# Performance work log

Measured on AMD Instinct MI355X. Metric: run time of the kernel, lower is better.

The kernel has to match this reference:

```python
import jax, jax.numpy as jnp
import numpy as np

NUM_STEPS = 5


def setup_inputs() -> dict:
    key = jax.random.key(0)
    ks = jax.random.split(key, 12)
    B, N, H, E, A = 8, 1024, 64, 2, 8
    initial_state = jax.random.normal(ks[0], (B, N, H), dtype=jnp.float32)
    annotation = jax.random.normal(ks[1], (B, N, A), dtype=jnp.float32)
    # sparse-ish positive adjacency, scaled so matmul outputs don't saturate gates
    adj_matrix = jax.random.uniform(ks[2], (B, N, 2 * N * E), dtype=jnp.float32) * 0.01
    s = 0.05
    W_edge = jax.random.normal(ks[3], (H, H * E), dtype=jnp.float32) * s
    b_edge = jax.random.normal(ks[4], (H * E,), dtype=jnp.float32) * s
    W_gate = jax.random.normal(ks[5], (3 * H, H), dtype=jnp.float32) * s
    b_gate = jax.random.normal(ks[6], (H,), dtype=jnp.float32) * s
    W_hid = jax.random.normal(ks[7], (H + A, H), dtype=jnp.float32) * s
    b_hid = jax.random.normal(ks[8], (H,), dtype=jnp.float32) * s
    W_out = jax.random.normal(ks[9], (H, 1), dtype=jnp.float32) * s
    b_out = jax.random.normal(ks[10], (1,), dtype=jnp.float32) * s
    return dict(initial_state=initial_state, annotation=annotation, adj_matrix=adj_matrix,
                W_edge=W_edge, b_edge=b_edge, W_gate=W_gate, b_gate=b_gate,
                W_hid=W_hid, b_hid=b_hid, W_out=W_out, b_out=b_out)


def reference(initial_state, annotation, adj_matrix, W_edge, b_edge,
              W_gate, b_gate, W_hid, b_hid, W_out, b_out):
    B, N, H = initial_state.shape
    E = W_edge.shape[1] // H
    boundary = N * E
    A_in = adj_matrix[:, :, :boundary]   # [B, N, N*E]
    A_out = adj_matrix[:, :, boundary:]  # [B, N, N*E]

    h = initial_state
    for _ in range(NUM_STEPS):
        # Linear(H, H*E) then view/transpose to [B, N*E, H].
        # Original computes incoming_edge and outgoing_edge with the SAME
        # linear on the SAME input -> identical tensors; compute once.
        edge = jnp.einsum('bnh,he->bne', h, W_edge) + b_edge      # [B, N, H*E]
        edge = edge.reshape(B, N, H, E).transpose(0, 3, 1, 2).reshape(B, N * E, H)
        a_in = jnp.matmul(A_in, edge)    # [B, N, H]
        a_out = jnp.matmul(A_out, edge)  # [B, N, H]
        a = jnp.concatenate([a_in, a_out, h], axis=2)             # [B, N, 3H]
        # update and reset use the same gate linear -> equal; compute once.
        z = jax.nn.sigmoid(jnp.einsum('bnk,kh->bnh', a, W_gate) + b_gate)
        a_r = jnp.concatenate([a_in, a_out, z * h], axis=2)
        h_tilde = jnp.tanh(jnp.einsum('bnk,kh->bnh', a_r, W_gate) + b_gate)
        h = (1.0 - z) * h + z * h_tilde

    # task_id not in {18, 19}: node-level output head
    ha = jnp.concatenate([h, annotation], axis=2)                 # [B, N, H+A]
    out = jnp.tanh(jnp.einsum('bnk,kh->bnh', ha, W_hid) + b_hid)  # [B, N, H]
    out = (jnp.einsum('bnh,ho->bno', out, W_out) + b_out).sum(axis=2)  # [B, N]
    return out
```

## Files before the change

### kernel.cpp

```cpp
#include <hip/hip_runtime.h>
#include <math.h>

#define BN    8
#define NN    1024
#define HH    64
#define ADIM  8
#define STEPS 5
#define K2    2048
#define ROWS  (BN*NN)

typedef __attribute__((ext_vector_type(8))) short bf16x8;
typedef __attribute__((ext_vector_type(4))) float f32x4;

__device__ __forceinline__ unsigned short f2bf(float f) {
    unsigned int u = __float_as_uint(f);
    u += 0x7FFF + ((u >> 16) & 1);
    return (unsigned short)(u >> 16);
}
__device__ __forceinline__ float bf2f(unsigned short h) {
    return __uint_as_float(((unsigned int)h) << 16);
}


__global__ __launch_bounds__(256) void conv_adj(
    const float* __restrict__ in, unsigned short* __restrict__ out)
{
    int tid = blockIdx.x * 256 + threadIdx.x;
    int r   = tid >> 7;
    int dkb = tid & 127;
    int b = r >> 10, n = r & 1023;
    int dir = dkb >> 6, kb = dkb & 63;
    const float* src = in + ((size_t)r << 12) + (dkb << 5);
    unsigned short* dst = out
        + ((((((size_t)b * 2 + dir) * 64 + kb) * 64 + (n >> 4)) << 4) + (n & 15)) * 32;
    #pragma unroll
    for (int i = 0; i < 8; ++i) {
        float4 v = ((const float4*)src)[i];
        ushort4 o;
        o.x = f2bf(v.x); o.y = f2bf(v.y); o.z = f2bf(v.z); o.w = f2bf(v.w);
        ((ushort4*)dst)[i] = o;
    }
}

__global__ __launch_bounds__(256) void prep_pack(
    const float* __restrict__ Wg, const float* __restrict__ We,
    unsigned short* __restrict__ wgp, unsigned short* __restrict__ wep)
{
    int t = blockIdx.x * 256 + threadIdx.x;
    if (t < 12288) {
        int k = t >> 6, c = t & 63;
        float v = Wg[t];
        unsigned short hi = f2bf(v);
        unsigned short lo = f2bf(v - bf2f(hi));
        wgp[(size_t)c * 192 + k] = hi;
        wgp[(size_t)(64 + c) * 192 + k] = lo;
    } else if (t < 20480) {
        int u = t - 12288;
        int k = u >> 7, c = u & 127;
        float v = We[u];
        unsigned short hi = f2bf(v);
        unsigned short lo = f2bf(v - bf2f(hi));
        wep[(size_t)c * 64 + k] = hi;
        wep[(size_t)(128 + c) * 64 + k] = lo;
    }
}

__device__ __forceinline__ size_t edge_addr(int b, int h, int k) {
    int kb = k >> 5, hb = h >> 4;
    return (((size_t)b * 64 + kb) * 4 + hb) * 512
         + (size_t)(h & 15) * 32 + (k & 31);
}

__global__ __launch_bounds__(256) void init_kernel(
    const float* __restrict__ init_state,
    const float* __restrict__ We, const float* __restrict__ be,
    float* __restrict__ h_ws, unsigned short* __restrict__ edge_t)
{
    __shared__ float h_lds[4][65];
    int t = threadIdx.x;
    int r = t >> 6, hp = t & 63;
    int row = blockIdx.x * 4 + r;
    float hv = init_state[(size_t)row * 64 + hp];
    h_ws[(size_t)row * 64 + hp] = hv;
    h_lds[r][hp] = hv;
    __syncthreads();
    int b = row >> 10, n = row & 1023;
    #pragma unroll
    for (int e = 0; e < 2; ++e) {
        float acc = be[hp * 2 + e];
        #pragma unroll 8
        for (int c = 0; c < 64; ++c)
            acc += h_lds[r][c] * We[c * 128 + hp * 2 + e];
        edge_t[edge_addr(b, hp, e * NN + n)] = f2bf(acc);
    }
}

__global__ __launch_bounds__(512) void step_kernel(
    const unsigned short* __restrict__ adjf,
    const unsigned short* __restrict__ ein,
    unsigned short* __restrict__ eout,
    float* __restrict__ h_ws,
    const unsigned short* __restrict__ wgp,
    const unsigned short* __restrict__ wep,
    const float* __restrict__ bg,
    const float* __restrict__ be,
    int do_edge)
{
    __shared__ __attribute__((aligned(16))) unsigned short Xhi[32][200];
    __shared__ __attribute__((aligned(16))) unsigned short Xlo[32][200];
    __shared__ __attribute__((aligned(16))) float          hf [32][68];
    __shared__ __attribute__((aligned(16))) unsigned short HNhi[32][72];
    __shared__ __attribute__((aligned(16))) unsigned short HNlo[32][72];
    __shared__ __attribute__((aligned(16))) float          red[4][16][68];

    int t  = threadIdx.x;
    int b  = blockIdx.x >> 5;
    int mt = blockIdx.x & 31;
    int n0 = mt * 32;
    size_t hbase = ((size_t)(b * NN + n0)) * 64;

    {
        int r = t >> 4, cg = (t & 15) * 4;
        float4 v = *(const float4*)(h_ws + hbase + (size_t)r * 64 + cg);
        float vv[4] = {v.x, v.y, v.z, v.w};
        #pragma unroll
        for (int j = 0; j < 4; ++j) {
            float hv = vv[j];
            unsigned short hi = f2bf(hv), lo = f2bf(hv - bf2f(hi));
            Xhi[r][128 + cg + j] = hi;
            Xlo[r][128 + cg + j] = lo;
            hf[r][cg + j] = hv;
        }
    }

    int lane = t & 63, w = t >> 6, l15 = lane & 15, q = lane >> 4;
    int dir = w >> 2, rh = (w >> 1) & 1, kc = w & 1;
    int nb  = mt * 2 + rh;
    int loff = l15 * 32 + q * 8;

    const unsigned short* Ap = adjf
        + ((((size_t)(b * 2 + dir) * 64 + kc * 32) * 64 + nb) * 512) + loff;
    const unsigned short* Bp = ein
        + (((size_t)b * 64 + kc * 32) * 4) * 512 + loff;

    f32x4 acc[4];
    #pragma unroll
    for (int ct = 0; ct < 4; ++ct) acc[ct] = (f32x4){0.f, 0.f, 0.f, 0.f};

    #pragma unroll 4
    for (int kb = 0; kb < 32; ++kb) {
        bf16x8 af = *(const bf16x8*)(Ap + kb * 32768);
        #pragma unroll
        for (int ct = 0; ct < 4; ++ct) {
            bf16x8 bfr = *(const bf16x8*)(Bp + kb * 2048 + ct * 512);
            acc[ct] = __builtin_amdgcn_mfma_f32_16x16x32_bf16(af, bfr, acc[ct], 0, 0, 0);
        }
    }

    int gg = w >> 1;
    if (kc == 1) {
        #pragma unroll
        for (int ct = 0; ct < 4; ++ct)
            #pragma unroll
            for (int i = 0; i < 4; ++i)
                red[gg][q * 4 + i][ct * 16 + l15] = acc[ct][i];
    }
    __syncthreads();
    if (kc == 0) {
        #pragma unroll
        for (int ct = 0; ct < 4; ++ct)
            #pragma unroll
            for (int i = 0; i < 4; ++i) {
                float v = acc[ct][i] + red[gg][q * 4 + i][ct * 16 + l15];
                unsigned short hi = f2bf(v), lo = f2bf(v - bf2f(hi));
                int r  = rh * 16 + q * 4 + i;
                int cc = dir * 64 + ct * 16 + l15;
                Xhi[r][cc] = hi;
                Xlo[r][cc] = lo;
            }
    }
    __syncthreads();

    int mg = w & 1, cg16 = w >> 1;
    int arow = mg * 16 + l15;
    int cc = cg16 * 16 + l15;
    const unsigned short* wcol = wgp + (size_t)cc * 192;
    f32x4 as = (f32x4){0.f, 0.f, 0.f, 0.f}, az;

    #pragma unroll
    for (int ks = 0; ks < 4; ++ks) {
        bf16x8 ah = *(const bf16x8*)&Xhi[arow][ks * 32 + q * 8];
        bf16x8 al = *(const bf16x8*)&Xlo[arow][ks * 32 + q * 8];
        const unsigned short* wb = wcol + ks * 32 + q * 8;
        bf16x8 bh = *(const bf16x8*)wb;
        bf16x8 bl = *(const bf16x8*)(wb + 64 * 192);
        as = __builtin_amdgcn_mfma_f32_16x16x32_bf16(ah, bh, as, 0, 0, 0);
        as = __builtin_amdgcn_mfma_f32_16x16x32_bf16(ah, bl, as, 0, 0, 0);
        as = __builtin_amdgcn_mfma_f32_16x16x32_bf16(al, bh, as, 0, 0, 0);
    }
    az = as;
    #pragma unroll
    for (int ks = 4; ks < 6; ++ks) {
        bf16x8 ah = *(const bf16x8*)&Xhi[arow][ks * 32 + q * 8];
        bf16x8 al = *(const bf16x8*)&Xlo[arow][ks * 32 + q * 8];
        const unsigned short* wb = wcol + ks * 32 + q * 8;
        bf16x8 bh = *(const bf16x8*)wb;
        bf16x8 bl = *(const bf16x8*)(wb + 64 * 192);
        az = __builtin_amdgcn_mfma_f32_16x16x32_bf16(ah, bh, az, 0, 0, 0);
        az = __builtin_amdgcn_mfma_f32_16x16x32_bf16(ah, bl, az, 0, 0, 0);
        az = __builtin_amdgcn_mfma_f32_16x16x32_bf16(al, bh, az, 0, 0, 0);
    }
    __syncthreads();

    float zv[4], hv[4];
    float bgv = bg[cc];
    #pragma unroll
    for (int i = 0; i < 4; ++i) {
        int r = mg * 16 + q * 4 + i;
        float z = 1.f / (1.f + __expf(-(az[i] + bgv)));
        float h = hf[r][cc];
        zv[i] = z; hv[i] = h;
        float zh = z * h;
        unsigned short hi = f2bf(zh), lo = f2bf(zh - bf2f(hi));
        Xhi[r][128 + cc] = hi;
        Xlo[r][128 + cc] = lo;
    }
    __syncthreads();

    #pragma unroll
    for (int ks = 4; ks < 6; ++ks) {
        bf16x8 ah = *(const bf16x8*)&Xhi[arow][ks * 32 + q * 8];
        bf16x8 al = *(const bf16x8*)&Xlo[arow][ks * 32 + q * 8];
        const unsigned short* wb = wcol + ks * 32 + q * 8;
        bf16x8 bh = *(const bf16x8*)wb;
        bf16x8 bl = *(const bf16x8*)(wb + 64 * 192);
        as = __builtin_amdgcn_mfma_f32_16x16x32_bf16(ah, bh, as, 0, 0, 0);
        as = __builtin_amdgcn_mfma_f32_16x16x32_bf16(ah, bl, as, 0, 0, 0);
        as = __builtin_amdgcn_mfma_f32_16x16x32_bf16(al, bh, as, 0, 0, 0);
    }

    #pragma unroll
    for (int i = 0; i < 4; ++i) {
        int r = mg * 16 + q * 4 + i;
        float ht = tanhf(as[i] + bgv);
        float z  = zv[i];
        float hn = (1.f - z) * hv[i] + z * ht;
        h_ws[hbase + (size_t)r * 64 + cc] = hn;
        if (do_edge) {
            unsigned short hi = f2bf(hn), lo = f2bf(hn - bf2f(hi));
            HNhi[r][cc] = hi;
            HNlo[r][cc] = lo;
        }
    }
    if (!do_edge) return;
    __syncthreads();

    int me = w & 1, cb2 = (w >> 1) * 2;
    int erow = me * 16 + l15;
    f32x4 ae[2];
    ae[0] = ae[1] = (f32x4){0.f, 0.f, 0.f, 0.f};
    #pragma unroll
    for (int ks = 0; ks < 2; ++ks) {
        bf16x8 ah = *(const bf16x8*)&HNhi[erow][ks * 32 + q * 8];
        bf16x8 al = *(const bf16x8*)&HNlo[erow][ks * 32 + q * 8];
        #pragma unroll
        for (int p = 0; p < 2; ++p) {
            int ec = (cb2 + p) * 16 + l15;
            const unsigned short* wb = wep + (size_t)ec * 64 + ks * 32 + q * 8;
            bf16x8 bh = *(const bf16x8*)wb;
            bf16x8 bl = *(const bf16x8*)(wb + 128 * 64);
            ae[p] = __builtin_amdgcn_mfma_f32_16x16x32_bf16(ah, bh, ae[p], 0, 0, 0);
            ae[p] = __builtin_amdgcn_mfma_f32_16x16x32_bf16(ah, bl, ae[p], 0, 0, 0);
            ae[p] = __builtin_amdgcn_mfma_f32_16x16x32_bf16(al, bh, ae[p], 0, 0, 0);
        }
    }
    #pragma unroll
    for (int p = 0; p < 2; ++p) {
        int ec = (cb2 + p) * 16 + l15;
        float bev = be[ec];
        int h = ec >> 1, e = ec & 1;
        int k = e * NN + n0 + me * 16 + q * 4;
        ushort4 ev;
        ev.x = f2bf(ae[p][0] + bev);
        ev.y = f2bf(ae[p][1] + bev);
        ev.z = f2bf(ae[p][2] + bev);
        ev.w = f2bf(ae[p][3] + bev);
        *(ushort4*)(eout + edge_addr(b, h, k)) = ev;
    }
}

__global__ __launch_bounds__(256) void head_kernel(
    const float* __restrict__ h_ws, const float* __restrict__ ann,
    const float* __restrict__ Wh, const float* __restrict__ bh,
    const float* __restrict__ Wo, const float* __restrict__ bo,
    float* __restrict__ out)
{
    __shared__ float Wh_l[72 * 64];
    __shared__ float ha[4][72];
    int t = threadIdx.x;
    #pragma unroll
    for (int l = 0; l < 18; ++l) {
        int idx = t + l * 256;
        Wh_l[idx] = Wh[idx];
    }
    int r = t >> 6, hp = t & 63;
    int row = blockIdx.x * 4 + r;
    ha[r][hp] = h_ws[(size_t)row * 64 + hp];
    if (hp < ADIM) ha[r][64 + hp] = ann[(size_t)row * ADIM + hp];
    __syncthreads();

    float acc = bh[hp];
    #pragma unroll 8
    for (int k = 0; k < 72; ++k)
        acc += ha[r][k] * Wh_l[k * 64 + hp];
    float v = tanhf(acc) * Wo[hp];
    #pragma unroll
    for (int o = 32; o; o >>= 1) v += __shfl_down(v, o, 64);
    if (hp == 0) out[row] = v + bo[0];
}

extern "C" void kernel_launch(void* const* d_in, const int* in_sizes, int n_in,
                              void* d_out, int out_size, void* d_ws, size_t ws_size,
                              hipStream_t stream) {
    const float* init_state = (const float*)d_in[0];
    const float* ann = (const float*)d_in[1];
    const float* adj = (const float*)d_in[2];
    const float* We  = (const float*)d_in[3];
    const float* be  = (const float*)d_in[4];
    const float* Wg  = (const float*)d_in[5];
    const float* bg  = (const float*)d_in[6];
    const float* Wh  = (const float*)d_in[7];
    const float* bh  = (const float*)d_in[8];
    const float* Wo  = (const float*)d_in[9];
    const float* bo  = (const float*)d_in[10];
    float* out = (float*)d_out;

    char* wsb = (char*)d_ws;
    unsigned short* adj_f  = (unsigned short*)wsb;
    unsigned short* edge_a = (unsigned short*)(wsb + 67108864);
    unsigned short* edge_b = (unsigned short*)(wsb + 69206016);
    float*          h_ws   = (float*)(wsb + 71303168);
    unsigned short* wgp    = (unsigned short*)(wsb + 73400320);
    unsigned short* wep    = (unsigned short*)(wsb + 73449472);

    conv_adj<<<dim3(4096), dim3(256), 0, stream>>>(adj, adj_f);
    prep_pack<<<dim3(80), dim3(256), 0, stream>>>(Wg, We, wgp, wep);
    init_kernel<<<dim3(ROWS / 4), dim3(256), 0, stream>>>(init_state, We, be, h_ws, edge_a);
    for (int s = 0; s < STEPS; ++s) {
        const unsigned short* ein = (s & 1) ? edge_b : edge_a;
        unsigned short* eo        = (s & 1) ? edge_a : edge_b;
        step_kernel<<<dim3(256), dim3(512), 0, stream>>>(
            adj_f, ein, eo, h_ws, wgp, wep, bg, be, (s < STEPS - 1) ? 1 : 0);
    }
    head_kernel<<<dim3(ROWS / 4), dim3(256), 0, stream>>>(h_ws, ann, Wh, bh, Wo, bo, out);
}
```

Before: 429.8 us.

## Merge prep kernels, fuse head into last step, use row-major adjacency layout

Combines the adjacency conversion, weight packing and initial edge computation into one launch, and fuses the output head into the final GRU step so h no longer round-trips through global memory for a separate head kernel. The adjacency bf16 copy moves from a tiled MFMA-fragment layout to plain row-major, which makes the conversion a straight streaming cast but gives the step kernel strided per-row fragment loads instead of contiguous tile loads. tanhf is swapped for an exp-based fast tanh. The trade-off is launch-count and layout-transform savings against possibly worse load coalescing in the main matmul loop.

```diff
diff --git a/kernel.cpp b/kernel.cpp
--- a/kernel.cpp
+++ b/kernel.cpp
@@ -20,83 +20,79 @@
 __device__ __forceinline__ float bf2f(unsigned short h) {
     return __uint_as_float(((unsigned int)h) << 16);
 }
-
-
-__global__ __launch_bounds__(256) void conv_adj(
-    const float* __restrict__ in, unsigned short* __restrict__ out)
-{
-    int tid = blockIdx.x * 256 + threadIdx.x;
-    int r   = tid >> 7;
-    int dkb = tid & 127;
-    int b = r >> 10, n = r & 1023;
-    int dir = dkb >> 6, kb = dkb & 63;
-    const float* src = in + ((size_t)r << 12) + (dkb << 5);
-    unsigned short* dst = out
-        + ((((((size_t)b * 2 + dir) * 64 + kb) * 64 + (n >> 4)) << 4) + (n & 15)) * 32;
-    #pragma unroll
-    for (int i = 0; i < 8; ++i) {
-        float4 v = ((const float4*)src)[i];
-        ushort4 o;
-        o.x = f2bf(v.x); o.y = f2bf(v.y); o.z = f2bf(v.z); o.w = f2bf(v.w);
-        ((ushort4*)dst)[i] = o;
-    }
-}
-
-__global__ __launch_bounds__(256) void prep_pack(
-    const float* __restrict__ Wg, const float* __restrict__ We,
-    unsigned short* __restrict__ wgp, unsigned short* __restrict__ wep)
-{
-    int t = blockIdx.x * 256 + threadIdx.x;
-    if (t < 12288) {
-        int k = t >> 6, c = t & 63;
-        float v = Wg[t];
-        unsigned short hi = f2bf(v);
-        unsigned short lo = f2bf(v - bf2f(hi));
-        wgp[(size_t)c * 192 + k] = hi;
-        wgp[(size_t)(64 + c) * 192 + k] = lo;
-    } else if (t < 20480) {
-        int u = t - 12288;
-        int k = u >> 7, c = u & 127;
-        float v = We[u];
-        unsigned short hi = f2bf(v);
-        unsigned short lo = f2bf(v - bf2f(hi));
-        wep[(size_t)c * 64 + k] = hi;
-        wep[(size_t)(128 + c) * 64 + k] = lo;
-    }
-}
-
-__device__ __forceinline__ size_t edge_addr(int b, int h, int k) {
-    int kb = k >> 5, hb = h >> 4;
-    return (((size_t)b * 64 + kb) * 4 + hb) * 512
-         + (size_t)(h & 15) * 32 + (k & 31);
-}
-
-__global__ __launch_bounds__(256) void init_kernel(
+__device__ __forceinline__ float ftanh(float x) {
+    float e = __expf(2.f * x);
+    return 1.f - 2.f / (e + 1.f);
+}
+
+__global__ __launch_bounds__(256) void pre_kernel(
+    const float* __restrict__ adj,
     const float* __restrict__ init_state,
     const float* __restrict__ We, const float* __restrict__ be,
-    float* __restrict__ h_ws, unsigned short* __restrict__ edge_t)
+    const float* __restrict__ Wg,
+    unsigned short* __restrict__ adjb,
+    unsigned short* __restrict__ edge_t,
+    float* __restrict__ h_ws,
+    unsigned short* __restrict__ wgp,
+    unsigned short* __restrict__ wep)
 {
     __shared__ float h_lds[4][65];
+    int bid = blockIdx.x;
     int t = threadIdx.x;
-    int r = t >> 6, hp = t & 63;
-    int row = blockIdx.x * 4 + r;
-    float hv = init_state[(size_t)row * 64 + hp];
-    h_ws[(size_t)row * 64 + hp] = hv;
-    h_lds[r][hp] = hv;
-    __syncthreads();
-    int b = row >> 10, n = row & 1023;
-    #pragma unroll
-    for (int e = 0; e < 2; ++e) {
-        float acc = be[hp * 2 + e];
-        #pragma unroll 8
-        for (int c = 0; c < 64; ++c)
-            acc += h_lds[r][c] * We[c * 128 + hp * 2 + e];
-        edge_t[edge_addr(b, hp, e * NN + n)] = f2bf(acc);
+
+    if (bid < 8192) {
+        int tid = bid * 256 + t;
+        #pragma unroll
+        for (int i = 0; i < 4; ++i) {
+            size_t idx = (size_t)tid + (size_t)i * 2097152;
+            float4 v = ((const float4*)adj)[idx];
+            ushort4 o;
+            o.x = f2bf(v.x); o.y = f2bf(v.y); o.z = f2bf(v.z); o.w = f2bf(v.w);
+            ((ushort4*)adjb)[idx] = o;
+        }
+        return;
+    }
+    if (bid < 10240) {
+        int blk = bid - 8192;
+        int r = t >> 6, hp = t & 63;
+        int row = blk * 4 + r;
+        float hv = init_state[(size_t)row * 64 + hp];
+        h_ws[(size_t)row * 64 + hp] = hv;
+        h_lds[r][hp] = hv;
+        __syncthreads();
+        int b = row >> 10, n = row & 1023;
+        #pragma unroll
+        for (int e = 0; e < 2; ++e) {
+            float acc = be[hp * 2 + e];
+            #pragma unroll 8
+            for (int c = 0; c < 64; ++c)
+                acc += h_lds[r][c] * We[c * 128 + hp * 2 + e];
+            edge_t[((size_t)b * 64 + hp) * K2 + e * NN + n] = f2bf(acc);
+        }
+        return;
+    }
+    for (int idx = t; idx < 20480; idx += 256) {
+        if (idx < 12288) {
+            int k = idx >> 6, c = idx & 63;
+            float v = Wg[idx];
+            unsigned short hi = f2bf(v);
+            unsigned short lo = f2bf(v - bf2f(hi));
+            wgp[(size_t)c * 192 + k] = hi;
+            wgp[(size_t)(64 + c) * 192 + k] = lo;
+        } else {
+            int u = idx - 12288;
+            int k = u >> 7, c = u & 127;
+            float v = We[u];
+            unsigned short hi = f2bf(v);
+            unsigned short lo = f2bf(v - bf2f(hi));
+            wep[(size_t)c * 64 + k] = hi;
+            wep[(size_t)(128 + c) * 64 + k] = lo;
+        }
     }
 }
 
 __global__ __launch_bounds__(512) void step_kernel(
-    const unsigned short* __restrict__ adjf,
+    const unsigned short* __restrict__ adjb,
     const unsigned short* __restrict__ ein,
     unsigned short* __restrict__ eout,
     float* __restrict__ h_ws,
@@ -104,7 +100,11 @@
     const unsigned short* __restrict__ wep,
     const float* __restrict__ bg,
     const float* __restrict__ be,
-    int do_edge)
+    const float* __restrict__ ann,
+    const float* __restrict__ Wh, const float* __restrict__ bh,
+    const float* __restrict__ Wo, const float* __restrict__ bo,
+    float* __restrict__ out,
+    int mode)
 {
     __shared__ __attribute__((aligned(16))) unsigned short Xhi[32][200];
     __shared__ __attribute__((aligned(16))) unsigned short Xlo[32][200];
@@ -135,24 +135,22 @@
 
     int lane = t & 63, w = t >> 6, l15 = lane & 15, q = lane >> 4;
     int dir = w >> 2, rh = (w >> 1) & 1, kc = w & 1;
-    int nb  = mt * 2 + rh;
-    int loff = l15 * 32 + q * 8;
-
-    const unsigned short* Ap = adjf
-        + ((((size_t)(b * 2 + dir) * 64 + kc * 32) * 64 + nb) * 512) + loff;
-    const unsigned short* Bp = ein
-        + (((size_t)b * 64 + kc * 32) * 4) * 512 + loff;
+
+    const unsigned short* Al = adjb
+        + ((size_t)(b * NN + n0 + rh * 16 + l15)) * 4096 + dir * K2 + kc * 1024 + q * 8;
+    const unsigned short* Bl = ein
+        + ((size_t)b * 64 + l15) * K2 + kc * 1024 + q * 8;
 
     f32x4 acc[4];
     #pragma unroll
     for (int ct = 0; ct < 4; ++ct) acc[ct] = (f32x4){0.f, 0.f, 0.f, 0.f};
 
-    #pragma unroll 4
-    for (int kb = 0; kb < 32; ++kb) {
-        bf16x8 af = *(const bf16x8*)(Ap + kb * 32768);
+    #pragma unroll 8
+    for (int ks = 0; ks < 32; ++ks) {
+        bf16x8 af = *(const bf16x8*)(Al + ks * 32);
         #pragma unroll
         for (int ct = 0; ct < 4; ++ct) {
-            bf16x8 bfr = *(const bf16x8*)(Bp + kb * 2048 + ct * 512);
+            bf16x8 bfr = *(const bf16x8*)(Bl + (size_t)ct * 16 * K2 + ks * 32);
             acc[ct] = __builtin_amdgcn_mfma_f32_16x16x32_bf16(af, bfr, acc[ct], 0, 0, 0);
         }
     }
@@ -174,9 +172,9 @@
                 float v = acc[ct][i] + red[gg][q * 4 + i][ct * 16 + l15];
                 unsigned short hi = f2bf(v), lo = f2bf(v - bf2f(hi));
                 int r  = rh * 16 + q * 4 + i;
-                int cc = dir * 64 + ct * 16 + l15;
-                Xhi[r][cc] = hi;
-                Xlo[r][cc] = lo;
+                int cc2 = dir * 64 + ct * 16 + l15;
+                Xhi[r][cc2] = hi;
+                Xlo[r][cc2] = lo;
             }
     }
     __syncthreads();
@@ -192,11 +190,11 @@
         bf16x8 ah = *(const bf16x8*)&Xhi[arow][ks * 32 + q * 8];
         bf16x8 al = *(const bf16x8*)&Xlo[arow][ks * 32 + q * 8];
         const unsigned short* wb = wcol + ks * 32 + q * 8;
-        bf16x8 bh = *(const bf16x8*)wb;
-        bf16x8 bl = *(const bf16x8*)(wb + 64 * 192);
-        as = __builtin_amdgcn_mfma_f32_16x16x32_bf16(ah, bh, as, 0, 0, 0);
-        as = __builtin_amdgcn_mfma_f32_16x16x32_bf16(ah, bl, as, 0, 0, 0);
-        as = __builtin_amdgcn_mfma_f32_16x16x32_bf16(al, bh, as, 0, 0, 0);
+        bf16x8 bh2 = *(const bf16x8*)wb;
+        bf16x8 bl2 = *(const bf16x8*)(wb + 64 * 192);
+        as = __builtin_amdgcn_mfma_f32_16x16x32_bf16(ah, bh2, as, 0, 0, 0);
+        as = __builtin_amdgcn_mfma_f32_16x16x32_bf16(ah, bl2, as, 0, 0, 0);
+        as = __builtin_amdgcn_mfma_f32_16x16x32_bf16(al, bh2, as, 0, 0, 0);
     }
     az = as;
     #pragma unroll
@@ -204,11 +202,11 @@
         bf16x8 ah = *(const bf16x8*)&Xhi[arow][ks * 32 + q * 8];
         bf16x8 al = *(const bf16x8*)&Xlo[arow][ks * 32 + q * 8];
         const unsigned short* wb = wcol + ks * 32 + q * 8;
-        bf16x8 bh = *(const bf16x8*)wb;
-        bf16x8 bl = *(const bf16x8*)(wb + 64 * 192);
-        az = __builtin_amdgcn_mfma_f32_16x16x32_bf16(ah, bh, az, 0, 0, 0);
-        az = __builtin_amdgcn_mfma_f32_16x16x32_bf16(ah, bl, az, 0, 0, 0);
-        az = __builtin_amdgcn_mfma_f32_16x16x32_bf16(al, bh, az, 0, 0, 0);
+        bf16x8 bh2 = *(const bf16x8*)wb;
+        bf16x8 bl2 = *(const bf16x8*)(wb + 64 * 192);
+        az = __builtin_amdgcn_mfma_f32_16x16x32_bf16(ah, bh2, az, 0, 0, 0);
+        az = __builtin_amdgcn_mfma_f32_16x16x32_bf16(ah, bl2, az, 0, 0, 0);
+        az = __builtin_amdgcn_mfma_f32_16x16x32_bf16(al, bh2, az, 0, 0, 0);
     }
     __syncthreads();
 
@@ -232,91 +230,94 @@
         bf16x8 ah = *(const bf16x8*)&Xhi[arow][ks * 32 + q * 8];
         bf16x8 al = *(const bf16x8*)&Xlo[arow][ks * 32 + q * 8];
         const unsigned short* wb = wcol + ks * 32 + q * 8;
-        bf16x8 bh = *(const bf16x8*)wb;
-        bf16x8 bl = *(const bf16x8*)(wb + 64 * 192);
-        as = __builtin_amdgcn_mfma_f32_16x16x32_bf16(ah, bh, as, 0, 0, 0);
-        as = __builtin_amdgcn_mfma_f32_16x16x32_bf16(ah, bl, as, 0, 0, 0);
-        as = __builtin_amdgcn_mfma_f32_16x16x32_bf16(al, bh, as, 0, 0, 0);
+        bf16x8 bh2 = *(const bf16x8*)wb;
+        bf16x8 bl2 = *(const bf16x8*)(wb + 64 * 192);
+        as = __builtin_amdgcn_mfma_f32_16x16x32_bf16(ah, bh2, as, 0, 0, 0);
+        as = __builtin_amdgcn_mfma_f32_16x16x32_bf16(ah, bl2, as, 0, 0, 0);
+        as = __builtin_amdgcn_mfma_f32_16x16x32_bf16(al, bh2, as, 0, 0, 0);
     }
 
     #pragma unroll
     for (int i = 0; i < 4; ++i) {
         int r = mg * 16 + q * 4 + i;
-        float ht = tanhf(as[i] + bgv);
+        float ht = ftanh(as[i] + bgv);
         float z  = zv[i];
         float hn = (1.f - z) * hv[i] + z * ht;
-        h_ws[hbase + (size_t)r * 64 + cc] = hn;
-        if (do_edge) {
+        if (mode == 0) {
+            h_ws[hbase + (size_t)r * 64 + cc] = hn;
             unsigned short hi = f2bf(hn), lo = f2bf(hn - bf2f(hi));
             HNhi[r][cc] = hi;
             HNlo[r][cc] = lo;
-        }
-    }
-    if (!do_edge) return;
-    __syncthreads();
-
-    int me = w & 1, cb2 = (w >> 1) * 2;
-    int erow = me * 16 + l15;
-    f32x4 ae[2];
-    ae[0] = ae[1] = (f32x4){0.f, 0.f, 0.f, 0.f};
-    #pragma unroll
-    for (int ks = 0; ks < 2; ++ks) {
-        bf16x8 ah = *(const bf16x8*)&HNhi[erow][ks * 32 + q * 8];
-        bf16x8 al = *(const bf16x8*)&HNlo[erow][ks * 32 + q * 8];
+        } else {
+            hf[r][cc] = hn;
+        }
+    }
+    __syncthreads();
+
+    if (mode == 0) {
+        int me = w & 1, cb2 = (w >> 1) * 2;
+        int erow = me * 16 + l15;
+        f32x4 ae[2];
+        ae[0] = ae[1] = (f32x4){0.f, 0.f, 0.f, 0.f};
+        #pragma unroll
+        for (int ks = 0; ks < 2; ++ks) {
+            bf16x8 ah = *(const bf16x8*)&HNhi[erow][ks * 32 + q * 8];
+            bf16x8 al = *(const bf16x8*)&HNlo[erow][ks * 32 + q * 8];
+            #pragma unroll
+            for (int p = 0; p < 2; ++p) {
+                int ec = (cb2 + p) * 16 + l15;
+                const unsigned short* wb = wep + (size_t)ec * 64 + ks * 32 + q * 8;
+                bf16x8 bh2 = *(const bf16x8*)wb;
+                bf16x8 bl2 = *(const bf16x8*)(wb + 128 * 64);
+                ae[p] = __builtin_amdgcn_mfma_f32_16x16x32_bf16(ah, bh2, ae[p], 0, 0, 0);
+                ae[p] = __builtin_amdgcn_mfma_f32_16x16x32_bf16(ah, bl2, ae[p], 0, 0, 0);
+                ae[p] = __builtin_amdgcn_mfma_f32_16x16x32_bf16(al, bh2, ae[p], 0, 0, 0);
+            }
+        }
         #pragma unroll
         for (int p = 0; p < 2; ++p) {
             int ec = (cb2 + p) * 16 + l15;
-            const unsigned short* wb = wep + (size_t)ec * 64 + ks * 32 + q * 8;
-            bf16x8 bh = *(const bf16x8*)wb;
-            bf16x8 bl = *(const bf16x8*)(wb + 128 * 64);
-            ae[p] = __builtin_amdgcn_mfma_f32_16x16x32_bf16(ah, bh, ae[p], 0, 0, 0);
-            ae[p] = __builtin_amdgcn_mfma_f32_16x16x32_bf16(ah, bl, ae[p], 0, 0, 0);
-            ae[p] = __builtin_amdgcn_mfma_f32_16x16x32_bf16(al, bh, ae[p], 0, 0, 0);
-        }
-    }
-    #pragma unroll
-    for (int p = 0; p < 2; ++p) {
-        int ec = (cb2 + p) * 16 + l15;
-        float bev = be[ec];
-        int h = ec >> 1, e = ec & 1;
-        int k = e * NN + n0 + me * 16 + q * 4;
-        ushort4 ev;
-        ev.x = f2bf(ae[p][0] + bev);
-        ev.y = f2bf(ae[p][1] + bev);
-        ev.z = f2bf(ae[p][2] + bev);
-        ev.w = f2bf(ae[p][3] + bev);
-        *(ushort4*)(eout + edge_addr(b, h, k)) = ev;
-    }
-}
-
-__global__ __launch_bounds__(256) void head_kernel(
-    const float* __restrict__ h_ws, const float* __restrict__ ann,
-    const float* __restrict__ Wh, const float* __restrict__ bh,
-    const float* __restrict__ Wo, const float* __restrict__ bo,
-    float* __restrict__ out)
-{
-    __shared__ float Wh_l[72 * 64];
-    __shared__ float ha[4][72];
-    int t = threadIdx.x;
-    #pragma unroll
-    for (int l = 0; l < 18; ++l) {
-        int idx = t + l * 256;
-        Wh_l[idx] = Wh[idx];
-    }
-    int r = t >> 6, hp = t & 63;
-    int row = blockIdx.x * 4 + r;
-    ha[r][hp] = h_ws[(size_t)row * 64 + hp];
-    if (hp < ADIM) ha[r][64 + hp] = ann[(size_t)row * ADIM + hp];
-    __syncthreads();
-
-    float acc = bh[hp];
-    #pragma unroll 8
-    for (int k = 0; k < 72; ++k)
-        acc += ha[r][k] * Wh_l[k * 64 + hp];
-    float v = tanhf(acc) * Wo[hp];
-    #pragma unroll
-    for (int o = 32; o; o >>= 1) v += __shfl_down(v, o, 64);
-    if (hp == 0) out[row] = v + bo[0];
+            float bev = be[ec];
+            int hp2 = ec >> 1, e = ec & 1;
+            size_t ebase = ((size_t)b * 64 + hp2) * K2 + (size_t)e * NN
+                         + n0 + me * 16 + q * 4;
+            ushort4 ev;
+            ev.x = f2bf(ae[p][0] + bev);
+            ev.y = f2bf(ae[p][1] + bev);
+            ev.z = f2bf(ae[p][2] + bev);
+            ev.w = f2bf(ae[p][3] + bev);
+            *(ushort4*)(eout + ebase) = ev;
+        }
+    } else {
+        int r = t >> 4, hq = (t & 15) * 4;
+        int row = b * NN + n0 + r;
+        float av[ADIM];
+        #pragma unroll
+        for (int j = 0; j < ADIM; ++j) av[j] = ann[(size_t)row * ADIM + j];
+        float ac2[4];
+        #pragma unroll
+        for (int i = 0; i < 4; ++i) ac2[i] = bh[hq + i];
+        #pragma unroll 8
+        for (int k = 0; k < 64; ++k) {
+            float hv2 = hf[r][k];
+            float4 wv = *(const float4*)&Wh[k * 64 + hq];
+            ac2[0] += hv2 * wv.x; ac2[1] += hv2 * wv.y;
+            ac2[2] += hv2 * wv.z; ac2[3] += hv2 * wv.w;
+        }
+        #pragma unroll
+        for (int k = 0; k < ADIM; ++k) {
+            float4 wv = *(const float4*)&Wh[(64 + k) * 64 + hq];
+            ac2[0] += av[k] * wv.x; ac2[1] += av[k] * wv.y;
+            ac2[2] += av[k] * wv.z; ac2[3] += av[k] * wv.w;
+        }
+        float v = 0.f;
+        #pragma unroll
+        for (int i = 0; i < 4; ++i)
+            v += ftanh(ac2[i]) * Wo[hq + i];
+        #pragma unroll
+        for (int m = 8; m; m >>= 1) v += __shfl_xor(v, m, 64);
+        if ((t & 15) == 0) out[row] = v + bo[0];
+    }
 }
 
 extern "C" void kernel_launch(void* const* d_in, const int* in_sizes, int n_in,
@@ -336,21 +337,20 @@
     float* out = (float*)d_out;
 
     char* wsb = (char*)d_ws;
-    unsigned short* adj_f  = (unsigned short*)wsb;
+    unsigned short* adjb   = (unsigned short*)wsb;
     unsigned short* edge_a = (unsigned short*)(wsb + 67108864);
     unsigned short* edge_b = (unsigned short*)(wsb + 69206016);
     float*          h_ws   = (float*)(wsb + 71303168);
     unsigned short* wgp    = (unsigned short*)(wsb + 73400320);
     unsigned short* wep    = (unsigned short*)(wsb + 73449472);
 
-    conv_adj<<<dim3(4096), dim3(256), 0, stream>>>(adj, adj_f);
-    prep_pack<<<dim3(80), dim3(256), 0, stream>>>(Wg, We, wgp, wep);
-    init_kernel<<<dim3(ROWS / 4), dim3(256), 0, stream>>>(init_state, We, be, h_ws, edge_a);
+    pre_kernel<<<dim3(10241), dim3(256), 0, stream>>>(
+        adj, init_state, We, be, Wg, adjb, edge_a, h_ws, wgp, wep);
     for (int s = 0; s < STEPS; ++s) {
         const unsigned short* ein = (s & 1) ? edge_b : edge_a;
         unsigned short* eo        = (s & 1) ? edge_a : edge_b;
         step_kernel<<<dim3(256), dim3(512), 0, stream>>>(
-            adj_f, ein, eo, h_ws, wgp, wep, bg, be, (s < STEPS - 1) ? 1 : 0);
-    }
-    head_kernel<<<dim3(ROWS / 4), dim3(256), 0, stream>>>(h_ws, ann, Wh, bh, Wo, bo, out);
-}
+            adjb, ein, eo, h_ws, wgp, wep, bg, be,
+            ann, Wh, bh, Wo, bo, out, (s == STEPS - 1) ? 1 : 0);
+    }
+}
```

New measurement: 523.2 us. +21.7%, slower.
